# Optimization experiments

Measured on AMD Instinct MI355X. Metric: run time of the kernel, lower is better.

Reference implementation:

```python
import jax, jax.numpy as jnp
from jax import lax
import numpy as np

WS = 5  # window_size
H = 6   # hidden_size
IN = 3 * WS  # 15
OUT = 2


def setup_inputs() -> dict:
    key = jax.random.key(0)
    k1, k2, k3, k4, k5 = jax.random.split(key, 5)
    B, T = 8192, 1024
    one_full_traj = jax.random.normal(k1, (B, T, 3), dtype=jnp.float32)
    # nn.Linear-style params: y = x @ W.T + b
    W1 = jax.random.normal(k2, (H, IN), dtype=jnp.float32) * (1.0 / np.sqrt(IN))
    b1 = jax.random.normal(k3, (H,), dtype=jnp.float32) * 0.05
    W2 = jax.random.normal(k4, (OUT, H), dtype=jnp.float32) * (1.0 / np.sqrt(H))
    b2 = jax.random.normal(k5, (OUT,), dtype=jnp.float32) * 0.05
    return {"one_full_traj": one_full_traj, "W1": W1, "b1": b1, "W2": W2, "b2": b2}


def reference(one_full_traj, W1, b1, W2, b2):
    ws = WS
    B, T, _ = one_full_traj.shape

    def mlp(x):  # [B, 3*ws] -> [B, 2]
        return jnp.tanh(x @ W1.T + b1) @ W2.T + b2

    def make_inp(seq):  # [B, ws, 3] -> [B, 3*ws], channel-major per original cat order
        return jnp.transpose(seq, (0, 2, 1)).reshape(B, 3 * ws)

    # step 0
    out = mlp(make_inp(one_full_traj[:, :ws, :]))[:, None, :]  # [B, 1, 2]

    # warm-up loop t = 1 .. ws-1 (small fixed Python loop, matches original indexing)
    for t in range(1, ws):
        n = out.shape[1]  # == t
        tmp = jnp.concatenate(
            [one_full_traj[:, ws + (t - 1):ws + (t - 1) + n, 0:1], out], axis=2
        )  # [B, t, 3]
        seq = jnp.concatenate([one_full_traj[:, t:ws, :], tmp], axis=1)  # [B, ws, 3]
        out = jnp.concatenate([out, mlp(make_inp(seq))[:, None, :]], axis=1)

    # sliding window of the last ws predictions as carry.
    u = one_full_traj[:, :, 0]  # control channel, [B, T]

    def step(win, t):
        uw = lax.dynamic_slice_in_dim(u, t, ws, axis=1)  # [B, ws]
        seq = jnp.concatenate([uw[:, :, None], win], axis=2)  # [B, ws, 3]
        pred = mlp(make_inp(seq))  # [B, 2]
        win = jnp.concatenate([win[:, 1:, :], pred[:, None, :]], axis=1)
        return win, pred

    ts = jnp.arange(ws, T - ws)
    _, preds = lax.scan(step, out, ts)  # preds: [T-2*ws, B, 2]
    return jnp.concatenate([out, jnp.transpose(preds, (1, 0, 2))], axis=1)  # [B, T-ws, 2]
```

## Files before the change

### kernel.cpp

```cpp
#include <hip/hip_runtime.h>
#include <math.h>

#define TLEN  1024
#define NSTEP 1019

template <int CTRL>
__device__ __forceinline__ float dpp_add(float v) {
    union { int i; float f; } in, out;
    in.f = v;
    out.i = __builtin_amdgcn_update_dpp(0, in.i, CTRL, 0xF, 0xF, false);
    return v + out.f;
}
__device__ __forceinline__ float sum8(float v) {
    v = dpp_add<0xB1>(v);
    v = dpp_add<0x4E>(v);
    v = dpp_add<0x141>(v);
    return v;
}
__device__ __forceinline__ float xhalf(float v) {
    union { int i; float f; } in, out;
    in.f = v;
    out.i = __builtin_amdgcn_update_dpp(0, in.i, 0x128, 0xF, 0xF, false);
    return out.f;
}

__device__ __forceinline__ float fast_exp2(float z) {
#if __has_builtin(__builtin_amdgcn_exp2f)
    return __builtin_amdgcn_exp2f(z);
#else
    return exp2f(z);
#endif
}

__global__ __launch_bounds__(64) void MLP_or_nextstep_kernel(
    const float* __restrict__ traj,
    const float* __restrict__ W1,
    const float* __restrict__ b1,
    const float* __restrict__ W2,
    const float* __restrict__ b2,
    float* __restrict__ out)
{
    __shared__ float lds_u[TLEN][4];

    const int lane = threadIdx.x;
    const int e    = lane >> 4;
    const int h    = (lane >> 3) & 1;
    const int n    = lane & 7;
    const int nh   = lane & 15;
    const int bstart = blockIdx.x * 4;
    const int b = bstart + e;

    const float* __restrict__ base = traj + (size_t)b * (TLEN * 3);
    float2* outb = (float2*)out + (size_t)b * NSTEP;
    const bool is_store_lane = (nh == 0);
    const bool stl  = (h == 0);
    const bool hsel = (h == 1);

    {
        const int s_elem = lane & 3;
        const int s_row  = lane >> 2;
        const float* __restrict__ sbase = traj + (size_t)(bstart + s_elem) * (TLEN * 3);
        for (int j = 0; j < TLEN / 16; ++j) {
            const float* gp = sbase + (size_t)(16 * j + s_row) * 3;
            __builtin_amdgcn_global_load_lds(
                (const __attribute__((address_space(1))) void*)gp,
                (__attribute__((address_space(3))) void*)&lds_u[16 * j][0],
                4, 0, 0);
        }
    }

    const float KK = 2.8853900817779268f;
    const int nr = (n < 6) ? n : 5;
    float w1row[15], b1r;
#pragma unroll
    for (int j = 0; j < 15; ++j) w1row[j] = KK * W1[nr * 15 + j];
    b1r = KK * b1[nr];
    const float w2_l  = (n < 6) ? W2[h * 6 + n] : 0.0f;
    const float bias  = (n == 6) ? b2[h] : 0.0f;
    const float c1 = -2.0f * w2_l, c0 = w2_l + bias;

    auto mlp = [&](const float* __restrict__ x, float& ya, float& yb) {
        float z0 = w1row[0] * x[0];
        float z1 = w1row[5] * x[5];
        float z2 = fmaf(w1row[10], x[10], b1r);
#pragma unroll
        for (int j = 1; j < 5; ++j) {
            z0 = fmaf(w1row[j],      x[j],      z0);
            z1 = fmaf(w1row[5 + j],  x[5 + j],  z1);
            z2 = fmaf(w1row[10 + j], x[10 + j], z2);
        }
        float z = (z0 + z1) + z2;
        float r = __builtin_amdgcn_rcpf(fast_exp2(z) + 1.0f);
        float own = sum8(fmaf(c1, r, c0));
        float oth = xhalf(own);
        ya = hsel ? oth : own;
        yb = hsel ? own : oth;
    };

    float uu[12], vv[5], wc[5];
#pragma unroll
    for (int i = 0; i < 12; ++i) uu[i] = base[i * 3];
#pragma unroll
    for (int i = 0; i < 5; ++i) { vv[i] = base[i * 3 + 1]; wc[i] = base[i * 3 + 2]; }

    float pa[5], pb[5];
    {
        float x[15] = {uu[0],uu[1],uu[2],uu[3],uu[4],
                       vv[0],vv[1],vv[2],vv[3],vv[4],
                       wc[0],wc[1],wc[2],wc[3],wc[4]};
        mlp(x, pa[0], pb[0]);
    }
    {
        float x[15] = {uu[1],uu[2],uu[3],uu[4],uu[5],
                       vv[1],vv[2],vv[3],vv[4],pa[0],
                       wc[1],wc[2],wc[3],wc[4],pb[0]};
        mlp(x, pa[1], pb[1]);
    }
    {
        float x[15] = {uu[2],uu[3],uu[4],uu[6],uu[7],
                       vv[2],vv[3],vv[4],pa[0],pa[1],
                       wc[2],wc[3],wc[4],pb[0],pb[1]};
        mlp(x, pa[2], pb[2]);
    }
    {
        float x[15] = {uu[3],uu[4],uu[7],uu[8],uu[9],
                       vv[3],vv[4],pa[0],pa[1],pa[2],
                       wc[3],wc[4],pb[0],pb[1],pb[2]};
        mlp(x, pa[3], pb[3]);
    }
    {
        float x[15] = {uu[4],uu[8],uu[9],uu[10],uu[11],
                       vv[4],pa[0],pa[1],pa[2],pa[3],
                       wc[4],pb[0],pb[1],pb[2],pb[3]};
        mlp(x, pa[4], pb[4]);
    }
    if (is_store_lane) {
#pragma unroll
        for (int i = 0; i < 5; ++i) outb[i] = make_float2(pa[i], pb[i]);
    }

    __syncthreads();

    float aw[5], bw[5];
#pragma unroll
    for (int i = 0; i < 5; ++i) { aw[i] = pa[i]; bw[i] = pb[i]; }

    const float* up  = &lds_u[5][e];
    const float* upn;
    float2* sp = outb + n + 5;
    float unA[9], unB[9];

#pragma unroll
    for (int i = 0; i < 9; ++i) unA[i] = up[4 * i];
    upn = up + 20;

#define LOADN(BUF)                                                           \
    {                                                                        \
        _Pragma("unroll")                                                    \
        for (int i = 0; i < 9; ++i) BUF[i] = upn[4 * i];                     \
        upn += 20;                                                           \
    }

    float duC[5], duD[5];
#pragma unroll
    for (int i = 0; i < 5; ++i) {
        float d = w1row[0] * unA[i];
        d = fmaf(w1row[1], unA[i + 1], d);
        d = fmaf(w1row[2], unA[i + 2], d);
        d = fmaf(w1row[3], unA[i + 3], d);
        d = fmaf(w1row[4], unA[i + 4], d);
        duC[i] = d;
    }

    LOADN(unB)

    float pAc, pBc, pAn, pBn;
    pAc = w1row[5] * aw[0];
    pAc = fmaf(w1row[6], aw[1], pAc);
    pAc = fmaf(w1row[7], aw[2], pAc);
    pAc = fmaf(w1row[8], aw[3], pAc);
    pBc = fmaf(w1row[10], bw[0], b1r);
    pBc = fmaf(w1row[11], bw[1], pBc);
    pBc = fmaf(w1row[12], bw[2], pBc);
    pBc = fmaf(w1row[13], bw[3], pBc);

#define STEP(S, DUC, DUN, UN, J, M)                                          \
    {                                                                        \
        float tA = fmaf(w1row[9],  aw[((S) + 4) % 5], pAc);                  \
        float tB = fmaf(w1row[14], bw[((S) + 4) % 5], pBc);                  \
        float z  = (DUC[S] + tA) + tB;                                       \
        float ex = fast_exp2(z);                                             \
             \
        pAn = w1row[5] * aw[((S) + 1) % 5];                                  \
        pAn = fmaf(w1row[6], aw[((S) + 2) % 5], pAn);                        \
        pAn = fmaf(w1row[7], aw[((S) + 3) % 5], pAn);                        \
        pAn = fmaf(w1row[8], aw[((S) + 4) % 5], pAn);                        \
        pBn = fmaf(w1row[10], bw[((S) + 1) % 5], b1r);                       \
        pBn = fmaf(w1row[11], bw[((S) + 2) % 5], pBn);                       \
        pBn = fmaf(w1row[12], bw[((S) + 3) % 5], pBn);                       \
        pBn = fmaf(w1row[13], bw[((S) + 4) % 5], pBn);                       \
        {                                                                    \
            float d = w1row[0] * UN[S];                                      \
            d = fmaf(w1row[1], UN[(S) + 1], d);                              \
            d = fmaf(w1row[2], UN[(S) + 2], d);                              \
            d = fmaf(w1row[3], UN[(S) + 3], d);                              \
            d = fmaf(w1row[4], UN[(S) + 4], d);                              \
            DUN[S] = d;                                                      \
        }                                                                    \
                                        \
        float r  = __builtin_amdgcn_rcpf(ex + 1.0f);                         \
        float own = sum8(fmaf(c1, r, c0));                                   \
        float oth = xhalf(own);                                              \
        float ya = hsel ? oth : own;                                         \
        float yb = hsel ? own : oth;                                         \
        if (nh == (J)) { ka##M = ya; kb##M = yb; }                           \
        aw[(S) % 5] = ya; bw[(S) % 5] = yb;                                  \
        pAc = pAn; pBc = pBn;                                                \
    }

#define STORE(M) if (stl) sp[8 * (M)] = make_float2(ka##M, kb##M);

    for (int sb = 0; sb < 25; ++sb) {
        float ka0 = 0, kb0 = 0, ka1 = 0, kb1 = 0, ka2 = 0, kb2 = 0,
              ka3 = 0, kb3 = 0, ka4 = 0, kb4 = 0;
        LOADN(unA)
        STEP(0, duC, duD, unB, 0, 0) STEP(1, duC, duD, unB, 1, 0) STEP(2, duC, duD, unB, 2, 0)
        STEP(3, duC, duD, unB, 3, 0) STEP(4, duC, duD, unB, 4, 0)
        LOADN(unB)
        STEP(0, duD, duC, unA, 5, 0) STEP(1, duD, duC, unA, 6, 0) STEP(2, duD, duC, unA, 7, 0) STORE(0)
        STEP(3, duD, duC, unA, 0, 1) STEP(4, duD, duC, unA, 1, 1)
        LOADN(unA)
        STEP(0, duC, duD, unB, 2, 1) STEP(1, duC, duD, unB, 3, 1) STEP(2, duC, duD, unB, 4, 1)
        STEP(3, duC, duD, unB, 5, 1) STEP(4, duC, duD, unB, 6, 1)
        LOADN(unB)
        STEP(0, duD, duC, unA, 7, 1) STORE(1)
        STEP(1, duD, duC, unA, 0, 2) STEP(2, duD, duC, unA, 1, 2) STEP(3, duD, duC, unA, 2, 2) STEP(4, duD, duC, unA, 3, 2)
        LOADN(unA)
        STEP(0, duC, duD, unB, 4, 2) STEP(1, duC, duD, unB, 5, 2) STEP(2, duC, duD, unB, 6, 2)
        STEP(3, duC, duD, unB, 7, 2) STORE(2)
        STEP(4, duC, duD, unB, 0, 3)
        LOADN(unB)
        STEP(0, duD, duC, unA, 1, 3) STEP(1, duD, duC, unA, 2, 3) STEP(2, duD, duC, unA, 3, 3)
        STEP(3, duD, duC, unA, 4, 3) STEP(4, duD, duC, unA, 5, 3)
        LOADN(unA)
        STEP(0, duC, duD, unB, 6, 3) STEP(1, duC, duD, unB, 7, 3) STORE(3)
        STEP(2, duC, duD, unB, 0, 4) STEP(3, duC, duD, unB, 1, 4) STEP(4, duC, duD, unB, 2, 4)
        LOADN(unB)
        STEP(0, duD, duC, unA, 3, 4) STEP(1, duD, duC, unA, 4, 4) STEP(2, duD, duC, unA, 5, 4)
        STEP(3, duD, duC, unA, 6, 4) STEP(4, duD, duC, unA, 7, 4) STORE(4)

        sp += 40;
    }

    float2* tp = outb + 1005;
#define TSTEP(S, UN, K)                                                      \
    {                                                                        \
        float z0 = w1row[0] * UN[S];                                         \
        float z1 = w1row[5] * aw[(S) % 5];                                   \
        float z2 = fmaf(w1row[10], bw[(S) % 5], b1r);                        \
        z0 = fmaf(w1row[1], UN[(S) + 1], z0);                                \
        z1 = fmaf(w1row[6], aw[((S) + 1) % 5], z1);                          \
        z2 = fmaf(w1row[11], bw[((S) + 1) % 5], z2);                         \
        z0 = fmaf(w1row[2], UN[(S) + 2], z0);                                \
        z1 = fmaf(w1row[7], aw[((S) + 2) % 5], z1);                          \
        z2 = fmaf(w1row[12], bw[((S) + 2) % 5], z2);                         \
        z0 = fmaf(w1row[3], UN[(S) + 3], z0);                                \
        z1 = fmaf(w1row[8], aw[((S) + 3) % 5], z1);                          \
        z2 = fmaf(w1row[13], bw[((S) + 3) % 5], z2);                         \
        z0 = fmaf(w1row[4], UN[(S) + 4], z0);                                \
        z1 = fmaf(w1row[9], aw[((S) + 4) % 5], z1);                          \
        z2 = fmaf(w1row[14], bw[((S) + 4) % 5], z2);                         \
        float z = (z0 + z1) + z2;                                            \
        float r = __builtin_amdgcn_rcpf(fast_exp2(z) + 1.0f);                \
        float own = sum8(fmaf(c1, r, c0));                                   \
        float oth = xhalf(own);                                              \
        float ya = hsel ? oth : own;                                         \
        float yb = hsel ? own : oth;                                         \
        if (is_store_lane) tp[K] = make_float2(ya, yb);                      \
        aw[(S) % 5] = ya; bw[(S) % 5] = yb;                                  \
    }

    TSTEP(0, unA, 0) TSTEP(1, unA, 1) TSTEP(2, unA, 2) TSTEP(3, unA, 3) TSTEP(4, unA, 4)
    LOADN(unA)
    TSTEP(0, unB, 5) TSTEP(1, unB, 6) TSTEP(2, unB, 7) TSTEP(3, unB, 8) TSTEP(4, unB, 9)
    TSTEP(0, unA, 10) TSTEP(1, unA, 11) TSTEP(2, unA, 12) TSTEP(3, unA, 13)

#undef TSTEP
#undef STORE
#undef STEP
#undef LOADN
}

extern "C" void kernel_launch(void* const* d_in, const int* in_sizes, int n_in,
                              void* d_out, int out_size, void* d_ws, size_t ws_size,
                              hipStream_t stream) {
    const float* traj = (const float*)d_in[0];
    const float* W1   = (const float*)d_in[1];
    const float* b1   = (const float*)d_in[2];
    const float* W2   = (const float*)d_in[3];
    const float* b2   = (const float*)d_in[4];
    float* out = (float*)d_out;

    const int grid = 8192 / 4;
    MLP_or_nextstep_kernel<<<grid, 64, 0, stream>>>(traj, W1, b1, W2, b2, out);
}
```

Before: 274.4 us.

## Split hidden pre-activation across lane halves, each half tracking one output channel

Each 8-lane half now holds only one of the two recurrent output channels. The first-layer dot product is split so one half computes the control-input plus channel-A terms and the other computes the channel-B terms plus bias. A DPP row-shift add combines the halves before the tanh, and each half reduces its own output without a cross-half exchange or select. This shortens the per-step serial FMA chain on the recurrent dependency and removes the select operations. In exchange it adds a DPP combine on the critical path before the exp, and stores become scalar floats per channel.

```diff
diff --git a/kernel.cpp b/kernel.cpp
--- a/kernel.cpp
+++ b/kernel.cpp
@@ -17,11 +17,8 @@
     v = dpp_add<0x141>(v);
     return v;
 }
-__device__ __forceinline__ float xhalf(float v) {
-    union { int i; float f; } in, out;
-    in.f = v;
-    out.i = __builtin_amdgcn_update_dpp(0, in.i, 0x128, 0xF, 0xF, false);
-    return out.f;
+__device__ __forceinline__ float comb16(float v) {
+    return dpp_add<0x128>(v);
 }
 
 __device__ __forceinline__ float fast_exp2(float z) {
@@ -44,17 +41,13 @@
 
     const int lane = threadIdx.x;
     const int e    = lane >> 4;
-    const int h    = (lane >> 3) & 1;
+    const int kk   = (lane >> 3) & 1;
     const int n    = lane & 7;
-    const int nh   = lane & 15;
     const int bstart = blockIdx.x * 4;
     const int b = bstart + e;
 
     const float* __restrict__ base = traj + (size_t)b * (TLEN * 3);
-    float2* outb = (float2*)out + (size_t)b * NSTEP;
-    const bool is_store_lane = (nh == 0);
-    const bool stl  = (h == 0);
-    const bool hsel = (h == 1);
+    float* outf = out + (size_t)b * (NSTEP * 2);
 
     {
         const int s_elem = lane & 3;
@@ -71,83 +64,65 @@
 
     const float KK = 2.8853900817779268f;
     const int nr = (n < 6) ? n : 5;
-    float w1row[15], b1r;
+    float w1row[15];
 #pragma unroll
     for (int j = 0; j < 15; ++j) w1row[j] = KK * W1[nr * 15 + j];
-    b1r = KK * b1[nr];
-    const float w2_l  = (n < 6) ? W2[h * 6 + n] : 0.0f;
-    const float bias  = (n == 6) ? b2[h] : 0.0f;
+    const float b1r = KK * b1[nr];
+    float wu[5], wh[5];
+#pragma unroll
+    for (int j = 0; j < 5; ++j) {
+        wu[j] = kk ? 0.0f : w1row[j];
+        wh[j] = kk ? w1row[10 + j] : w1row[5 + j];
+    }
+    const float seed = kk ? b1r : 0.0f;
+    const float w2_l = (n < 6) ? W2[kk * 6 + n] : 0.0f;
+    const float bias = (n == 6) ? b2[kk] : 0.0f;
     const float c1 = -2.0f * w2_l, c0 = w2_l + bias;
 
-    auto mlp = [&](const float* __restrict__ x, float& ya, float& yb) {
-        float z0 = w1row[0] * x[0];
-        float z1 = w1row[5] * x[5];
-        float z2 = fmaf(w1row[10], x[10], b1r);
-#pragma unroll
-        for (int j = 1; j < 5; ++j) {
-            z0 = fmaf(w1row[j],      x[j],      z0);
-            z1 = fmaf(w1row[5 + j],  x[5 + j],  z1);
-            z2 = fmaf(w1row[10 + j], x[10 + j], z2);
+    float h[5];
+    float uu[12];
+#pragma unroll
+    for (int i = 0; i < 12; ++i) uu[i] = base[i * 3];
+#pragma unroll
+    for (int i = 0; i < 5; ++i) h[i] = base[i * 3 + 1 + kk];
+
+    auto wstep = [&](float x0, float x1, float x2, float x3, float x4) -> float {
+        float zh = fmaf(wh[0], h[0], seed);
+        zh = fmaf(wh[1], h[1], zh);
+        zh = fmaf(wh[2], h[2], zh);
+        zh = fmaf(wh[3], h[3], zh);
+        zh = fmaf(wh[4], h[4], zh);
+        float du = wu[0] * x0;
+        du = fmaf(wu[1], x1, du);
+        du = fmaf(wu[2], x2, du);
+        du = fmaf(wu[3], x3, du);
+        du = fmaf(wu[4], x4, du);
+        float zp = du + zh;
+        float z  = comb16(zp);
+        float r  = __builtin_amdgcn_rcpf(fast_exp2(z) + 1.0f);
+        float y  = sum8(fmaf(c1, r, c0));
+        h[0] = h[1]; h[1] = h[2]; h[2] = h[3]; h[3] = h[4]; h[4] = y;
+        return y;
+    };
+
+    {
+        float pv[5];
+        pv[0] = wstep(uu[0], uu[1], uu[2], uu[3], uu[4]);
+        pv[1] = wstep(uu[1], uu[2], uu[3], uu[4], uu[5]);
+        pv[2] = wstep(uu[2], uu[3], uu[4], uu[6], uu[7]);
+        pv[3] = wstep(uu[3], uu[4], uu[7], uu[8], uu[9]);
+        pv[4] = wstep(uu[4], uu[8], uu[9], uu[10], uu[11]);
+        if (n == 0) {
+#pragma unroll
+            for (int i = 0; i < 5; ++i) outf[2 * i + kk] = pv[i];
         }
-        float z = (z0 + z1) + z2;
-        float r = __builtin_amdgcn_rcpf(fast_exp2(z) + 1.0f);
-        float own = sum8(fmaf(c1, r, c0));
-        float oth = xhalf(own);
-        ya = hsel ? oth : own;
-        yb = hsel ? own : oth;
-    };
-
-    float uu[12], vv[5], wc[5];
-#pragma unroll
-    for (int i = 0; i < 12; ++i) uu[i] = base[i * 3];
-#pragma unroll
-    for (int i = 0; i < 5; ++i) { vv[i] = base[i * 3 + 1]; wc[i] = base[i * 3 + 2]; }
-
-    float pa[5], pb[5];
-    {
-        float x[15] = {uu[0],uu[1],uu[2],uu[3],uu[4],
-                       vv[0],vv[1],vv[2],vv[3],vv[4],
-                       wc[0],wc[1],wc[2],wc[3],wc[4]};
-        mlp(x, pa[0], pb[0]);
-    }
-    {
-        float x[15] = {uu[1],uu[2],uu[3],uu[4],uu[5],
-                       vv[1],vv[2],vv[3],vv[4],pa[0],
-                       wc[1],wc[2],wc[3],wc[4],pb[0]};
-        mlp(x, pa[1], pb[1]);
-    }
-    {
-        float x[15] = {uu[2],uu[3],uu[4],uu[6],uu[7],
-                       vv[2],vv[3],vv[4],pa[0],pa[1],
-                       wc[2],wc[3],wc[4],pb[0],pb[1]};
-        mlp(x, pa[2], pb[2]);
-    }
-    {
-        float x[15] = {uu[3],uu[4],uu[7],uu[8],uu[9],
-                       vv[3],vv[4],pa[0],pa[1],pa[2],
-                       wc[3],wc[4],pb[0],pb[1],pb[2]};
-        mlp(x, pa[3], pb[3]);
-    }
-    {
-        float x[15] = {uu[4],uu[8],uu[9],uu[10],uu[11],
-                       vv[4],pa[0],pa[1],pa[2],pa[3],
-                       wc[4],pb[0],pb[1],pb[2],pb[3]};
-        mlp(x, pa[4], pb[4]);
-    }
-    if (is_store_lane) {
-#pragma unroll
-        for (int i = 0; i < 5; ++i) outb[i] = make_float2(pa[i], pb[i]);
     }
 
     __syncthreads();
-
-    float aw[5], bw[5];
-#pragma unroll
-    for (int i = 0; i < 5; ++i) { aw[i] = pa[i]; bw[i] = pb[i]; }
 
     const float* up  = &lds_u[5][e];
     const float* upn;
-    float2* sp = outb + n + 5;
+    float* spf = outf + (n + 5) * 2 + kk;
     float unA[9], unB[9];
 
 #pragma unroll
@@ -164,65 +139,54 @@
     float duC[5], duD[5];
 #pragma unroll
     for (int i = 0; i < 5; ++i) {
-        float d = w1row[0] * unA[i];
-        d = fmaf(w1row[1], unA[i + 1], d);
-        d = fmaf(w1row[2], unA[i + 2], d);
-        d = fmaf(w1row[3], unA[i + 3], d);
-        d = fmaf(w1row[4], unA[i + 4], d);
+        float d = wu[0] * unA[i];
+        d = fmaf(wu[1], unA[i + 1], d);
+        d = fmaf(wu[2], unA[i + 2], d);
+        d = fmaf(wu[3], unA[i + 3], d);
+        d = fmaf(wu[4], unA[i + 4], d);
         duC[i] = d;
     }
 
     LOADN(unB)
 
-    float pAc, pBc, pAn, pBn;
-    pAc = w1row[5] * aw[0];
-    pAc = fmaf(w1row[6], aw[1], pAc);
-    pAc = fmaf(w1row[7], aw[2], pAc);
-    pAc = fmaf(w1row[8], aw[3], pAc);
-    pBc = fmaf(w1row[10], bw[0], b1r);
-    pBc = fmaf(w1row[11], bw[1], pBc);
-    pBc = fmaf(w1row[12], bw[2], pBc);
-    pBc = fmaf(w1row[13], bw[3], pBc);
+    float pC, pN;
+    pC = fmaf(wh[0], h[0], seed);
+    pC = fmaf(wh[1], h[1], pC);
+    pC = fmaf(wh[2], h[2], pC);
+    pC = fmaf(wh[3], h[3], pC);
 
 #define STEP(S, DUC, DUN, UN, J, M)                                          \
     {                                                                        \
-        float tA = fmaf(w1row[9],  aw[((S) + 4) % 5], pAc);                  \
-        float tB = fmaf(w1row[14], bw[((S) + 4) % 5], pBc);                  \
-        float z  = (DUC[S] + tA) + tB;                                       \
-        float ex = fast_exp2(z);                                             \
-             \
-        pAn = w1row[5] * aw[((S) + 1) % 5];                                  \
-        pAn = fmaf(w1row[6], aw[((S) + 2) % 5], pAn);                        \
-        pAn = fmaf(w1row[7], aw[((S) + 3) % 5], pAn);                        \
-        pAn = fmaf(w1row[8], aw[((S) + 4) % 5], pAn);                        \
-        pBn = fmaf(w1row[10], bw[((S) + 1) % 5], b1r);                       \
-        pBn = fmaf(w1row[11], bw[((S) + 2) % 5], pBn);                       \
-        pBn = fmaf(w1row[12], bw[((S) + 3) % 5], pBn);                       \
-        pBn = fmaf(w1row[13], bw[((S) + 4) % 5], pBn);                       \
+        float t_  = fmaf(wh[4], h[((S) + 4) % 5], pC);                       \
+        float zp_ = DUC[S] + t_;                                             \
+        float z_  = comb16(zp_);                                             \
+        float ex_ = fast_exp2(z_);                                           \
+        pN = fmaf(wh[0], h[((S) + 1) % 5], seed);                            \
+        pN = fmaf(wh[1], h[((S) + 2) % 5], pN);                              \
+        pN = fmaf(wh[2], h[((S) + 3) % 5], pN);                              \
+        pN = fmaf(wh[3], h[((S) + 4) % 5], pN);                              \
         {                                                                    \
-            float d = w1row[0] * UN[S];                                      \
-            d = fmaf(w1row[1], UN[(S) + 1], d);                              \
-            d = fmaf(w1row[2], UN[(S) + 2], d);                              \
-            d = fmaf(w1row[3], UN[(S) + 3], d);                              \
-            d = fmaf(w1row[4], UN[(S) + 4], d);                              \
-            DUN[S] = d;                                                      \
+            float d_ = wu[0] * UN[S];                                        \
+            d_ = fmaf(wu[1], UN[(S) + 1], d_);                               \
+            d_ = fmaf(wu[2], UN[(S) + 2], d_);                               \
+            d_ = fmaf(wu[3], UN[(S) + 3], d_);                               \
+            d_ = fmaf(wu[4], UN[(S) + 4], d_);                               \
+            DUN[S] = d_;                                                     \
         }                                                                    \
-                                        \
-        float r  = __builtin_amdgcn_rcpf(ex + 1.0f);                         \
-        float own = sum8(fmaf(c1, r, c0));                                   \
-        float oth = xhalf(own);                                              \
-        float ya = hsel ? oth : own;                                         \
-        float yb = hsel ? own : oth;                                         \
-        if (nh == (J)) { ka##M = ya; kb##M = yb; }                           \
-        aw[(S) % 5] = ya; bw[(S) % 5] = yb;                                  \
-        pAc = pAn; pBc = pBn;                                                \
-    }
-
-#define STORE(M) if (stl) sp[8 * (M)] = make_float2(ka##M, kb##M);
+        float r_ = __builtin_amdgcn_rcpf(ex_ + 1.0f);                        \
+        float y_ = fmaf(c1, r_, c0);                                         \
+        y_ = dpp_add<0xB1>(y_);                                              \
+        y_ = dpp_add<0x4E>(y_);                                              \
+        y_ = dpp_add<0x141>(y_);                                             \
+        if (n == (J)) ks##M = y_;                                            \
+        h[(S) % 5] = y_;                                                     \
+        pC = pN;                                                             \
+    }
+
+#define STORE(M) spf[16 * (M)] = ks##M;
 
     for (int sb = 0; sb < 25; ++sb) {
-        float ka0 = 0, kb0 = 0, ka1 = 0, kb1 = 0, ka2 = 0, kb2 = 0,
-              ka3 = 0, kb3 = 0, ka4 = 0, kb4 = 0;
+        float ks0 = 0, ks1 = 0, ks2 = 0, ks3 = 0, ks4 = 0;
         LOADN(unA)
         STEP(0, duC, duD, unB, 0, 0) STEP(1, duC, duD, unB, 1, 0) STEP(2, duC, duD, unB, 2, 0)
         STEP(3, duC, duD, unB, 3, 0) STEP(4, duC, duD, unB, 4, 0)
@@ -249,35 +213,28 @@
         STEP(0, duD, duC, unA, 3, 4) STEP(1, duD, duC, unA, 4, 4) STEP(2, duD, duC, unA, 5, 4)
         STEP(3, duD, duC, unA, 6, 4) STEP(4, duD, duC, unA, 7, 4) STORE(4)
 
-        sp += 40;
-    }
-
-    float2* tp = outb + 1005;
+        spf += 80;
+    }
+
+    float* tpf = outf + 1005 * 2 + kk;
 #define TSTEP(S, UN, K)                                                      \
     {                                                                        \
-        float z0 = w1row[0] * UN[S];                                         \
-        float z1 = w1row[5] * aw[(S) % 5];                                   \
-        float z2 = fmaf(w1row[10], bw[(S) % 5], b1r);                        \
-        z0 = fmaf(w1row[1], UN[(S) + 1], z0);                                \
-        z1 = fmaf(w1row[6], aw[((S) + 1) % 5], z1);                          \
-        z2 = fmaf(w1row[11], bw[((S) + 1) % 5], z2);                         \
-        z0 = fmaf(w1row[2], UN[(S) + 2], z0);                                \
-        z1 = fmaf(w1row[7], aw[((S) + 2) % 5], z1);                          \
-        z2 = fmaf(w1row[12], bw[((S) + 2) % 5], z2);                         \
-        z0 = fmaf(w1row[3], UN[(S) + 3], z0);                                \
-        z1 = fmaf(w1row[8], aw[((S) + 3) % 5], z1);                          \
-        z2 = fmaf(w1row[13], bw[((S) + 3) % 5], z2);                         \
-        z0 = fmaf(w1row[4], UN[(S) + 4], z0);                                \
-        z1 = fmaf(w1row[9], aw[((S) + 4) % 5], z1);                          \
-        z2 = fmaf(w1row[14], bw[((S) + 4) % 5], z2);                         \
-        float z = (z0 + z1) + z2;                                            \
-        float r = __builtin_amdgcn_rcpf(fast_exp2(z) + 1.0f);                \
-        float own = sum8(fmaf(c1, r, c0));                                   \
-        float oth = xhalf(own);                                              \
-        float ya = hsel ? oth : own;                                         \
-        float yb = hsel ? own : oth;                                         \
-        if (is_store_lane) tp[K] = make_float2(ya, yb);                      \
-        aw[(S) % 5] = ya; bw[(S) % 5] = yb;                                  \
+        float zh_ = fmaf(wh[0], h[(S) % 5], seed);                           \
+        zh_ = fmaf(wh[1], h[((S) + 1) % 5], zh_);                            \
+        zh_ = fmaf(wh[2], h[((S) + 2) % 5], zh_);                            \
+        zh_ = fmaf(wh[3], h[((S) + 3) % 5], zh_);                            \
+        zh_ = fmaf(wh[4], h[((S) + 4) % 5], zh_);                            \
+        float d_ = wu[0] * UN[S];                                            \
+        d_ = fmaf(wu[1], UN[(S) + 1], d_);                                   \
+        d_ = fmaf(wu[2], UN[(S) + 2], d_);                                   \
+        d_ = fmaf(wu[3], UN[(S) + 3], d_);                                   \
+        d_ = fmaf(wu[4], UN[(S) + 4], d_);                                   \
+        float zp_ = d_ + zh_;                                                \
+        float z_  = comb16(zp_);                                             \
+        float r_ = __builtin_amdgcn_rcpf(fast_exp2(z_) + 1.0f);              \
+        float y_ = sum8(fmaf(c1, r_, c0));                                   \
+        if (n == 0) tpf[2 * (K)] = y_;                                       \
+        h[(S) % 5] = y_;                                                     \
     }
 
     TSTEP(0, unA, 0) TSTEP(1, unA, 1) TSTEP(2, unA, 2) TSTEP(3, unA, 3) TSTEP(4, unA, 4)
```

Result: faster. 237.2 us (-13.6%).
